# Optimization experiments

Hardware: AMD Instinct MI355X
Metric: run time of the kernel (lower is better)

## Reference

```python
import jax, jax.numpy as jnp
import numpy as np

N, K, C, G, B = 65536, 16, 64, 8, 4
PE_IN = 28  # 3 + 1 + 2*4*2 + 1*4*2
EPS = 1e-5
FREQS = (1.0, 2.0, 4.0, 8.0)  # 2 ** linspace(0, 3, 4)


def _bn(x, p):
    # inference-mode BatchNorm1d over last dim; p: [4, d] = (gamma, beta, mean, var)
    return (x - p[2]) * (p[0] / jnp.sqrt(p[3] + EPS)) + p[1]


def setup_inputs() -> dict:
    key = jax.random.key(0)
    ks = iter(jax.random.split(key, 48))

    def nrm(shape, s=0.05):
        return jax.random.normal(next(ks), shape, jnp.float32) * s

    def bnp(d):
        k1, k2, k3, k4 = jax.random.split(next(ks), 4)
        return jnp.stack([
            jax.random.uniform(k1, (d,), jnp.float32, 0.5, 1.5),   # gamma
            jax.random.normal(k2, (d,), jnp.float32) * 0.1,        # beta
            jax.random.normal(k3, (d,), jnp.float32) * 0.1,        # running mean
            jax.random.uniform(k4, (d,), jnp.float32, 0.5, 1.5),   # running var
        ])

    return dict(
        feat=nrm((N, C), 1.0),
        coord=jax.random.normal(next(ks), (N, 3), jnp.float32),
        reference_index=jax.random.randint(next(ks), (N, K), 0, N),
        offset=jnp.array([N // 4, N // 2, 3 * N // 4, N], dtype=jnp.int32),
        Wq=nrm((C, C)), bq=nrm((C,)), bnq=bnp(C),
        Wk=nrm((C, C)), bk=nrm((C,)), bnk=bnp(C),
        Wv=nrm((C, C)), bv=nrm((C,)),
        pe_W1=nrm((PE_IN, C)), pe_b1=nrm((C,)), pe_bn=bnp(C),
        pe_W2=nrm((C, C)), pe_b2=nrm((C,)),
        we_W1=nrm((C, G)), we_b1=nrm((G,)), we_bn=bnp(G),
        we_W2=nrm((G, G)), we_b2=nrm((G,)),
        cg_W1=nrm((3 * C, C)), cg_b1=nrm((C,)), cg_bn=bnp(C),
        cg_W2=nrm((C, G), 0.001), cg_b2=jnp.full((G,), 3.0, jnp.float32),
    )


def reference(feat, coord, reference_index, offset, Wq, bq, bnq, Wk, bk, bnk,
              Wv, bv, pe_W1, pe_b1, pe_bn, pe_W2, pe_b2,
              we_W1, we_b1, we_bn, we_W2, we_b2,
              cg_W1, cg_b1, cg_bn, cg_W2, cg_b2):
    n = feat.shape[0]
    q = jax.nn.relu(_bn(feat @ Wq + bq, bnq))          # [N, C]
    k = jax.nn.relu(_bn(feat @ Wk + bk, bnk))          # [N, C]
    v = feat @ Wv + bv                                 # [N, C]

    idx = reference_index                              # [N, K]; -1 = pad
    idx_safe = jnp.maximum(idx, 0)
    key_feat = k[idx_safe]                             # [N, K, C] gather
    neighbor_xyz = coord[idx_safe]                     # [N, K, 3]
    value_g = v[idx_safe]                              # [N, K, C]

    delta = neighbor_xyz - coord[:, None, :]           # [N, K, 3]
    # Anisotropic Fourier relative position encoding
    x = delta.reshape(-1, 3)
    d_xy, d_z = x[:, :2], x[:, 2:3]
    dist = jnp.linalg.norm(x, axis=1, keepdims=True)
    feats = [x, dist]
    for f in FREQS:
        feats += [jnp.sin(d_xy * (f * np.pi)), jnp.cos(d_xy * (f * np.pi))]
    for f in FREQS:
        feats += [jnp.sin(d_z * (f * np.pi)), jnp.cos(d_z * (f * np.pi))]
    xe = jnp.concatenate(feats, axis=1)                # [N*K, 28]
    rpe = jax.nn.relu(_bn(xe @ pe_W1 + pe_b1, pe_bn)) @ pe_W2 + pe_b2
    rpe = rpe.reshape(n, idx.shape[1], -1)             # [N, K, C]

    relation = key_feat - q[:, None, :] + rpe          # [N, K, C]
    geom_w = jax.nn.relu(_bn(relation @ we_W1 + we_b1, we_bn)) @ we_W2 + we_b2  # [N, K, G]

    neighbor_ctx = q[idx_safe].max(axis=1)             # [N, C]
    seg = jnp.searchsorted(offset, jnp.arange(n), side='right')
    seg_max = jax.ops.segment_max(q, seg, num_segments=offset.shape[0])
    global_ctx = seg_max[seg]                          # [N, C] offset-wise global max pool

    gate_in = jnp.concatenate([q, neighbor_ctx, global_ctx], axis=-1)  # [N, 3C]
    gate = jax.nn.sigmoid(
        jax.nn.relu(_bn(gate_in @ cg_W1 + cg_b1, cg_bn)) @ cg_W2 + cg_b2)  # [N, G]

    attn = jax.nn.softmax(geom_w * gate[:, None, :], axis=1)  # softmax over K
    mask = jnp.sign(idx + 1).astype(attn.dtype)        # [N, K]
    attn = attn * mask[:, :, None]

    vg = value_g.reshape(n, idx.shape[1], G, -1)       # [N, K, G, C//G]
    out = jnp.einsum('nkgi,nkg->ngi', vg, attn)
    return out.reshape(n, -1)
```

## Files before the change

### kernel.cpp

```cpp
#include <hip/hip_runtime.h>
#include <hip/hip_bf16.h>

#define EPSF 1e-5f

typedef __attribute__((ext_vector_type(8))) short short8;
typedef __attribute__((ext_vector_type(4))) float f32x4;

__device__ __forceinline__ int seg_of(int i, int o0, int o1, int o2) {
    return (i >= o0) + (i >= o1) + (i >= o2);
}

__device__ __forceinline__ unsigned short f2bf(float f) {
    unsigned int u = __float_as_uint(f);
    unsigned int r = (u + 0x7fffu + ((u >> 16) & 1u)) >> 16;
    return (unsigned short)r;
}
__device__ __forceinline__ unsigned int pack2bf(float a, float b) {
    return (unsigned int)f2bf(a) | ((unsigned int)f2bf(b) << 16);
}
__device__ __forceinline__ float bflo(unsigned int u) { return __uint_as_float(u << 16); }
__device__ __forceinline__ float bfhi(unsigned int u) { return __uint_as_float(u & 0xffff0000u); }

__device__ __forceinline__ void stage_rows_bf16(const unsigned short* __restrict__ src,
                                                unsigned short* dst, int l) {
    int row = l >> 2, cq = (l & 3) * 16;
    const short8* s = (const short8*)(src + (size_t)row*64 + cq);
    short8* d0 = (short8*)(dst + row*72 + cq);
    d0[0] = s[0];
    d0[1] = s[1];
}

__device__ __forceinline__ void stage_rows_f32(const float* __restrict__ src,
                                               unsigned short* dst, int l) {
    int row = l >> 2, cq = (l & 3) * 16;
    const float4* s = (const float4*)(src + (size_t)row*64 + cq);
    unsigned int* d = (unsigned int*)(dst + row*72 + cq);
    #pragma unroll
    for (int i = 0; i < 4; ++i) {
        float4 f = s[i];
        d[i*2]   = pack2bf(f.x, f.y);
        d[i*2+1] = pack2bf(f.z, f.w);
    }
}

__global__ __launch_bounds__(256) void k_prep(
    const float* __restrict__ pe_W1, const float* __restrict__ pe_b1, const float* __restrict__ pe_bn,
    const float* __restrict__ pe_W2, const float* __restrict__ pe_b2,
    const float* __restrict__ we_W1, const float* __restrict__ we_b1, const float* __restrict__ we_bn,
    const float* __restrict__ cg_W1, const float* __restrict__ cg_b1, const float* __restrict__ cg_bn,
    const float* __restrict__ Wq, const float* __restrict__ bq, const float* __restrict__ bnq,
    const float* __restrict__ Wk, const float* __restrict__ bk, const float* __restrict__ bnk,
    const float* __restrict__ Wv,
    float* __restrict__ peb1f, float* __restrict__ cvecg, float* __restrict__ cgb1f,
    float* __restrict__ biasqF, float* __restrict__ biaskF, float* __restrict__ cgW1cF,
    unsigned short* __restrict__ WqF, unsigned short* __restrict__ WkF, unsigned short* __restrict__ WvF,
    unsigned short* __restrict__ weW1F, unsigned short* __restrict__ cgW1aF,
    unsigned short* __restrict__ cgW1bF,
    unsigned short* __restrict__ W1frag, unsigned short* __restrict__ Wcfrag)
{
    int t = threadIdx.x;
    __shared__ float sc1[64], csc[64], sqv[64], skv[64], wsc[8], wsh[8];
    __shared__ float sWe[64][8], sWb[8], sWc[64][8];
    if (t < 64) {
        float g = pe_bn[t], b = pe_bn[64+t], m = pe_bn[128+t], v = pe_bn[192+t];
        float s = g / sqrtf(v + EPSF);
        sc1[t] = s; peb1f[t] = pe_b1[t]*s + (b - m*s);
        g = cg_bn[t]; b = cg_bn[64+t]; m = cg_bn[128+t]; v = cg_bn[192+t];
        s = g / sqrtf(v + EPSF);
        csc[t] = s; cgb1f[t] = cg_b1[t]*s + (b - m*s);
        g = bnq[t]; b = bnq[64+t]; m = bnq[128+t]; v = bnq[192+t];
        s = g / sqrtf(v + EPSF);
        sqv[t] = s; biasqF[t] = bq[t]*s + (b - m*s);
        g = bnk[t]; b = bnk[64+t]; m = bnk[128+t]; v = bnk[192+t];
        s = g / sqrtf(v + EPSF);
        skv[t] = s; biaskF[t] = bk[t]*s + (b - m*s);
    }
    if (t < 8) {
        float g = we_bn[t], b = we_bn[8+t], m = we_bn[16+t], v = we_bn[24+t];
        float s = g / sqrtf(v + EPSF);
        wsc[t] = s; wsh[t] = b - m*s;
    }
    __syncthreads();
    for (int u = t; u < 512; u += 256) { int g = u & 7; sWe[u >> 3][g] = we_W1[u] * wsc[g]; }
    if (t < 8) sWb[t] = we_b1[t] * wsc[t] + wsh[t];
    __syncthreads();
    for (int u = t; u < 512; u += 256) {
        int h = u >> 3, g = u & 7;
        float a = 0.f;
        for (int c = 0; c < 64; ++c) a += pe_W2[h*64 + c] * sWe[c][g];
        sWc[h][g] = a;
    }
    if (t < 8) {
        float a = sWb[t];
        for (int c = 0; c < 64; ++c) a += pe_b2[c] * sWe[c][t];
        cvecg[t] = a;
    }
    __syncthreads();
    for (int u = t; u < 4096; u += 256) {
        int tile = u >> 9, l = (u >> 3) & 63, j = u & 7;
        int col = (tile >> 1)*16 + (l & 15);
        int kk  = (tile & 1)*32 + (l >> 4)*8 + j;
        WqF[u]    = f2bf(Wq[kk*64 + col] * sqv[col]);
        WkF[u]    = f2bf(Wk[kk*64 + col] * skv[col]);
        WvF[u]    = f2bf(Wv[kk*64 + col]);
        cgW1aF[u] = f2bf(cg_W1[kk*64 + col] * csc[col]);
        cgW1bF[u] = f2bf(cg_W1[(64 + kk)*64 + col] * csc[col]);
    }
    for (int u = t; u < 1024; u += 256) {
        int tile = u >> 9, l = (u >> 3) & 63, j = u & 7;
        int col = l & 15;
        int kk  = tile*32 + (l >> 4)*8 + j;
        weW1F[u] = (col < 8) ? f2bf(sWe[kk][col]) : 0;
    }
    for (int u = t; u < 4096; u += 256) {
        int k = u >> 6, c = u & 63;
        cgW1cF[u] = cg_W1[(128 + k)*64 + c] * csc[c];
    }
    {
        int ct = t >> 6, l = t & 63;
        int col = 16*ct + (l & 15), kg = l >> 4;
        #pragma unroll
        for (int j = 0; j < 8; ++j) {
            int k = kg*8 + j;
            float v = (k < 28) ? pe_W1[k*64 + col] * sc1[col] : 0.f;
            W1frag[ct*512 + l*8 + j] = f2bf(v);
        }
    }
    if (t < 128) {
        int kg = t >> 6, l = t & 63, g = l & 15;
        #pragma unroll
        for (int j = 0; j < 8; ++j) {
            int k = kg*32 + (l >> 4)*8 + j;
            float v = (g < 8) ? sWc[k][g] : 0.f;
            Wcfrag[kg*512 + l*8 + j] = f2bf(v);
        }
    }
}

__global__ __launch_bounds__(256) void k_prep2(
    const float* __restrict__ cg_W2, const float* __restrict__ we_W2,
    unsigned short* __restrict__ cgW2F, unsigned short* __restrict__ W2frag)
{
    int t = threadIdx.x;
    for (int u = t; u < 1024; u += 256) {
        int tile = u >> 9, l = (u >> 3) & 63, j = u & 7;
        int col = l & 15;
        int kk  = tile*32 + (l >> 4)*8 + j;
        cgW2F[u] = (col < 8) ? f2bf(cg_W2[kk*8 + col]) : 0;
    }
    if (t < 64) {
        int l = t, g = l & 15;
        #pragma unroll
        for (int j = 0; j < 8; ++j) {
            float v = (l < 16 && g < 8) ? we_W2[j*8 + g] : 0.f;
            W2frag[l*8 + j] = f2bf(v);
        }
    }
}

__global__ __launch_bounds__(256) void k_qkv(
    const float* __restrict__ feat, const int* __restrict__ offs,
    const unsigned short* __restrict__ WqF, const unsigned short* __restrict__ WkF,
    const unsigned short* __restrict__ WvF, const unsigned short* __restrict__ weW1F,
    const float* __restrict__ biasqF, const float* __restrict__ biaskF,
    const float* __restrict__ bv,
    unsigned short* __restrict__ v_bf, unsigned short* __restrict__ q_bf,
    float* __restrict__ kw, float* __restrict__ qw, float* __restrict__ seg_max)
{
    __shared__ unsigned short sF[4][16*72];
    __shared__ unsigned short sQ[4][16*72];
    __shared__ unsigned short sK[4][16*72];
    __shared__ float sSeg[64];

    int t = threadIdx.x, w = t >> 6, l = t & 63;
    int lc = l & 15, lg = l >> 4;
    int rblk = blockIdx.x * 64;
    int r0 = rblk + w * 16;
    int o0 = offs[0], o1 = offs[1], o2 = offs[2];
    bool fast = seg_of(rblk, o0,o1,o2) == seg_of(rblk + 63, o0,o1,o2);

    if (t < 64) sSeg[t] = 0.f;
    __syncthreads();

    stage_rows_f32(feat + (size_t)r0*64, sF[w], l);
    short8 a0 = *(const short8*)(sF[w] + lc*72 + lg*8);
    short8 a1 = *(const short8*)(sF[w] + lc*72 + 32 + lg*8);

    float bqc[4], bkc[4], bvc[4];
    #pragma unroll
    for (int ct = 0; ct < 4; ++ct) {
        bqc[ct] = biasqF[ct*16 + lc];
        bkc[ct] = biaskF[ct*16 + lc];
        bvc[ct] = bv[ct*16 + lc];
    }

    #pragma unroll
    for (int ct = 0; ct < 4; ++ct) {
        f32x4 z = {0.f,0.f,0.f,0.f};
        short8 b0 = *(const short8*)(WqF + (ct*2+0)*512 + l*8);
        short8 b1 = *(const short8*)(WqF + (ct*2+1)*512 + l*8);
        f32x4 c = __builtin_amdgcn_mfma_f32_16x16x32_bf16(a0, b0, z, 0,0,0);
        c = __builtin_amdgcn_mfma_f32_16x16x32_bf16(a1, b1, c, 0,0,0);
        float cmax = 0.f;
        #pragma unroll
        for (int reg = 0; reg < 4; ++reg) {
            float qv = fmaxf(c[reg] + bqc[ct], 0.f);
            sQ[w][(lg*4 + reg)*72 + ct*16 + lc] = f2bf(qv);
            if (fast) cmax = fmaxf(cmax, qv);
            else atomicMax((unsigned int*)&seg_max[seg_of(r0 + lg*4 + reg,o0,o1,o2)*64 + ct*16 + lc],
                           __float_as_uint(qv));
        }
        if (fast) {
            cmax = fmaxf(cmax, __shfl_xor(cmax, 16));
            cmax = fmaxf(cmax, __shfl_xor(cmax, 32));
            if (lg == 0)
                atomicMax((unsigned int*)&sSeg[ct*16 + lc], __float_as_uint(cmax));
        }
    }
    #pragma unroll
    for (int ct = 0; ct < 4; ++ct) {
        f32x4 z = {0.f,0.f,0.f,0.f};
        short8 b0 = *(const short8*)(WkF + (ct*2+0)*512 + l*8);
        short8 b1 = *(const short8*)(WkF + (ct*2+1)*512 + l*8);
        f32x4 c = __builtin_amdgcn_mfma_f32_16x16x32_bf16(a0, b0, z, 0,0,0);
        c = __builtin_amdgcn_mfma_f32_16x16x32_bf16(a1, b1, c, 0,0,0);
        #pragma unroll
        for (int reg = 0; reg < 4; ++reg)
            sK[w][(lg*4 + reg)*72 + ct*16 + lc] = f2bf(fmaxf(c[reg] + bkc[ct], 0.f));
    }
    #pragma unroll
    for (int ct = 0; ct < 4; ++ct) {
        f32x4 z = {0.f,0.f,0.f,0.f};
        short8 b0 = *(const short8*)(WvF + (ct*2+0)*512 + l*8);
        short8 b1 = *(const short8*)(WvF + (ct*2+1)*512 + l*8);
        f32x4 c = __builtin_amdgcn_mfma_f32_16x16x32_bf16(a0, b0, z, 0,0,0);
        c = __builtin_amdgcn_mfma_f32_16x16x32_bf16(a1, b1, c, 0,0,0);
        #pragma unroll
        for (int reg = 0; reg < 4; ++reg)
            sF[w][(lg*4 + reg)*72 + ct*16 + lc] = f2bf(c[reg] + bvc[ct]);
    }
    {
        short8 wb0 = *(const short8*)(weW1F + l*8);
        short8 wb1 = *(const short8*)(weW1F + 512 + l*8);
        short8 aq0 = *(const short8*)(sQ[w] + lc*72 + lg*8);
        short8 aq1 = *(const short8*)(sQ[w] + lc*72 + 32 + lg*8);
        short8 ak0 = *(const short8*)(sK[w] + lc*72 + lg*8);
        short8 ak1 = *(const short8*)(sK[w] + lc*72 + 32 + lg*8);
        f32x4 z = {0.f,0.f,0.f,0.f};
        f32x4 cq = __builtin_amdgcn_mfma_f32_16x16x32_bf16(aq0, wb0, z, 0,0,0);
        cq = __builtin_amdgcn_mfma_f32_16x16x32_bf16(aq1, wb1, cq, 0,0,0);
        f32x4 ck = __builtin_amdgcn_mfma_f32_16x16x32_bf16(ak0, wb0, z, 0,0,0);
        ck = __builtin_amdgcn_mfma_f32_16x16x32_bf16(ak1, wb1, ck, 0,0,0);
        if (lc < 8) {
            #pragma unroll
            for (int reg = 0; reg < 4; ++reg) {
                qw[(size_t)(r0 + lg*4 + reg)*8 + lc] = cq[reg];
                kw[(size_t)(r0 + lg*4 + reg)*8 + lc] = ck[reg];
            }
        }
    }
    #pragma unroll
    for (int rep = 0; rep < 2; ++rep) {
        int row = (l >> 3) + rep*8;
        int ch = (l & 7) * 8;
        short8 vq = *(const short8*)(sQ[w] + row*72 + ch);
        *(short8*)(q_bf + (size_t)(r0 + row)*64 + ch) = vq;
        short8 vv = *(const short8*)(sF[w] + row*72 + ch);
        *(short8*)(v_bf + (size_t)(r0 + row)*64 + ch) = vv;
    }
    __syncthreads();
    if (fast && t < 64)
        atomicMax((unsigned int*)&seg_max[seg_of(rblk,o0,o1,o2)*64 + t],
                  __float_as_uint(sSeg[t]));
}

__global__ __launch_bounds__(256) void k_seg(
    const float* __restrict__ seg_max, const float* __restrict__ cgW1cF,
    const float* __restrict__ cgb1f, float* __restrict__ gseg2)
{
    int t = threadIdx.x;
    int c = t & 63, s = t >> 6;
    float a = cgb1f[c];
    for (int j = 0; j < 64; ++j) a += seg_max[s*64 + j] * cgW1cF[j*64 + c];
    gseg2[s*64 + c] = a;
}

__global__ __launch_bounds__(256, 3) void k_main(
    const float* __restrict__ coord, const int* __restrict__ ridx,
    const unsigned short* __restrict__ v_bf, const unsigned short* __restrict__ q_bf,
    const float* __restrict__ kw, const float* __restrict__ qw,
    const float* __restrict__ peb1f, const float* __restrict__ cvecg,
    const float* __restrict__ we_b2, const float* __restrict__ cg_b2,
    const float* __restrict__ gseg2, const int* __restrict__ offs,
    const unsigned short* __restrict__ W1frag, const unsigned short* __restrict__ Wcfrag,
    const unsigned short* __restrict__ W2frag,
    const unsigned short* __restrict__ cgW1aF, const unsigned short* __restrict__ cgW1bF,
    const unsigned short* __restrict__ cgW2F,
    float* __restrict__ out)
{
    __shared__ __align__(16) unsigned short sA1[256*40];
    __shared__ __align__(16) unsigned short sA2[4][16*72];
    __shared__ __align__(16) unsigned short sAh2[4][128];
    __shared__ float sAttn[4][4][16][9];
    __shared__ int sIds[256];
    __shared__ __align__(16) unsigned short sQg[16*72];
    __shared__ __align__(16) unsigned short sN[16*72];
    __shared__ __align__(16) unsigned short sHg[16*72];
    __shared__ float sGate[16][9];

    int t = threadIdx.x, w = t >> 6, l = t & 63;
    int lc = l & 15, lg = l >> 4;
    int n0 = blockIdx.x * 16;
    int o0 = offs[0], o1 = offs[1], o2 = offs[2];

    int id = ridx[(size_t)n0*16 + t];
    sIds[t] = id;
    int ids = max(id, 0);
    int nself = n0 + (t >> 4);
    {
        float cx = coord[nself*3], cy = coord[nself*3+1], cz = coord[nself*3+2];
        float dx = coord[ids*3]   - cx;
        float dy = coord[ids*3+1] - cy;
        float dz = coord[ids*3+2] - cz;
        float dist = sqrtf(dx*dx + dy*dy + dz*dz);
        unsigned int* row = (unsigned int*)sA1 + t*20;
        row[0] = pack2bf(dx, dy);
        row[1] = pack2bf(dz, dist);
        float sx, cx2, sy, cy2, sz, cz2;
        __sincosf(dx * 3.14159265358979f, &sx, &cx2);
        __sincosf(dy * 3.14159265358979f, &sy, &cy2);
        __sincosf(dz * 3.14159265358979f, &sz, &cz2);
        row[2]  = pack2bf(sx, sy);
        row[3]  = pack2bf(cx2, cy2);
        row[10] = pack2bf(sz, cz2);
        #pragma unroll
        for (int fi = 1; fi < 4; ++fi) {
            float nsx = 2.f*sx*cx2, ncx = fmaf(-2.f*sx, sx, 1.f);
            float nsy = 2.f*sy*cy2, ncy = fmaf(-2.f*sy, sy, 1.f);
            float nsz = 2.f*sz*cz2, ncz = fmaf(-2.f*sz, sz, 1.f);
            row[2 + 2*fi] = pack2bf(nsx, nsy);
            row[3 + 2*fi] = pack2bf(ncx, ncy);
            row[10 + fi]  = pack2bf(nsz, ncz);
            sx = nsx; cx2 = ncx; sy = nsy; cy2 = ncy; sz = nsz; cz2 = ncz;
        }
        row[14] = 0u; row[15] = 0u;
    }
    if (t < 64) stage_rows_bf16(q_bf + (size_t)n0*64, sQg, t);
    __syncthreads();

    {
        int p = t >> 4, s = t & 15;
        const int* ip = &sIds[p*16];
        float m0 = 0.f, m1 = 0.f, m2 = 0.f, m3 = 0.f;
        #pragma unroll
        for (int kb = 0; kb < 16; kb += 4) {
            uint2 u[4];
            #pragma unroll
            for (int j = 0; j < 4; ++j) {
                int idn = max(ip[kb + j], 0);
                u[j] = *(const uint2*)(q_bf + (size_t)idn*64 + s*4);
            }
            #pragma unroll
            for (int j = 0; j < 4; ++j) {
                m0 = fmaxf(m0, bflo(u[j].x)); m1 = fmaxf(m1, bfhi(u[j].x));
                m2 = fmaxf(m2, bflo(u[j].y)); m3 = fmaxf(m3, bfhi(u[j].y));
            }
        }
        unsigned int* d = (unsigned int*)(sN + p*72 + s*4);
        d[0] = pack2bf(m0, m1);
        d[1] = pack2bf(m2, m3);
    }
    __syncthreads();

    {
        short8 a0 = *(const short8*)(sQg + lc*72 + lg*8);
        short8 a1 = *(const short8*)(sQg + lc*72 + 32 + lg*8);
        short8 nv0 = *(const short8*)(sN + lc*72 + lg*8);
        short8 nv1 = *(const short8*)(sN + lc*72 + 32 + lg*8);
        f32x4 c4;
        #pragma unroll
        for (int reg = 0; reg < 4; ++reg)
            c4[reg] = gseg2[seg_of(n0 + lg*4 + reg, o0, o1, o2)*64 + w*16 + lc];
        short8 b0 = *(const short8*)(cgW1aF + (w*2+0)*512 + l*8);
        short8 b1 = *(const short8*)(cgW1aF + (w*2+1)*512 + l*8);
        c4 = __builtin_amdgcn_mfma_f32_16x16x32_bf16(a0, b0, c4, 0,0,0);
        c4 = __builtin_amdgcn_mfma_f32_16x16x32_bf16(a1, b1, c4, 0,0,0);
        short8 b2 = *(const short8*)(cgW1bF + (w*2+0)*512 + l*8);
        short8 b3 = *(const short8*)(cgW1bF + (w*2+1)*512 + l*8);
        c4 = __builtin_amdgcn_mfma_f32_16x16x32_bf16(nv0, b2, c4, 0,0,0);
        c4 = __builtin_amdgcn_mfma_f32_16x16x32_bf16(nv1, b3, c4, 0,0,0);
        #pragma unroll
        for (int reg = 0; reg < 4; ++reg)
            sHg[(lg*4 + reg)*72 + w*16 + lc] = f2bf(fmaxf(c4[reg], 0.f));
    }
    __syncthreads();

    if (w == 0) {
        short8 ah0 = *(const short8*)(sHg + lc*72 + lg*8);
        short8 ah1 = *(const short8*)(sHg + lc*72 + 32 + lg*8);
        short8 w0f = *(const short8*)(cgW2F + l*8);
        short8 w1f = *(const short8*)(cgW2F + 512 + l*8);
        float bg = cg_b2[lc & 7];
        f32x4 cg;
        #pragma unroll
        for (int reg = 0; reg < 4; ++reg) cg[reg] = bg;
        cg = __builtin_amdgcn_mfma_f32_16x16x32_bf16(ah0, w0f, cg, 0,0,0);
        cg = __builtin_amdgcn_mfma_f32_16x16x32_bf16(ah1, w1f, cg, 0,0,0);
        if (lc < 8) {
            #pragma unroll
            for (int reg = 0; reg < 4; ++reg)
                sGate[lg*4 + reg][lc] = 1.f / (1.f + __expf(-cg[reg]));
        }
    }
    __syncthreads();

    int g7 = lc & 7;
    short8 bW1[4], bWc[2], bW2;
    #pragma unroll
    for (int ct = 0; ct < 4; ++ct) bW1[ct] = *(const short8*)(W1frag + ct*512 + l*8);
    bWc[0] = *(const short8*)(Wcfrag + l*8);
    bWc[1] = *(const short8*)(Wcfrag + 512 + l*8);
    bW2 = *(const short8*)(W2frag + l*8);

    float bias1[4];
    #pragma unroll
    for (int ct = 0; ct < 4; ++ct) bias1[ct] = peb1f[16*ct + lc];
    float cvec_g = cvecg[g7];
    float bias3 = we_b2[g7];

    #pragma unroll
    for (int rt = 0; rt < 4; ++rt) {
        int n = n0 + w*4 + rt;
        short8 a1 = *(const short8*)(sA1 + (w*64 + rt*16 + lc)*40 + lg*8);
        f32x4 c1[4];
        #pragma unroll
        for (int ct = 0; ct < 4; ++ct) {
            f32x4 z = {0.f, 0.f, 0.f, 0.f};
            c1[ct] = __builtin_amdgcn_mfma_f32_16x16x32_bf16(a1, bW1[ct], z, 0, 0, 0);
        }
        #pragma unroll
        for (int ct = 0; ct < 4; ++ct) {
            #pragma unroll
            for (int reg = 0; reg < 4; ++reg) {
                float h1 = fmaxf(c1[ct][reg] + bias1[ct], 0.f);
                sA2[w][(lg*4 + reg)*72 + 16*ct + lc] = f2bf(h1);
            }
        }
        int ids_r[4];
        #pragma unroll
        for (int reg = 0; reg < 4; ++reg) ids_r[reg] = sIds[w*64 + rt*16 + lg*4 + reg];
        float qwv = qw[(size_t)n*8 + g7];
        f32x4 c2;
        #pragma unroll
        for (int reg = 0; reg < 4; ++reg)
            c2[reg] = kw[(size_t)max(ids_r[reg],0)*8 + g7] - qwv + cvec_g;
        short8 a20 = *(const short8*)(sA2[w] + lc*72 + lg*8);
        short8 a21 = *(const short8*)(sA2[w] + lc*72 + 32 + lg*8);
        c2 = __builtin_amdgcn_mfma_f32_16x16x32_bf16(a20, bWc[0], c2, 0, 0, 0);
        c2 = __builtin_amdgcn_mfma_f32_16x16x32_bf16(a21, bWc[1], c2, 0, 0, 0);
        if (lc < 8) {
            #pragma unroll
            for (int reg = 0; reg < 4; ++reg)
                sAh2[w][(lg*4 + reg)*8 + lc] = f2bf(fmaxf(c2[reg], 0.f));
        }
        short8 a3 = {0,0,0,0,0,0,0,0};
        if (l < 16) a3 = *(const short8*)(sAh2[w] + lc*8);
        f32x4 c3;
        #pragma unroll
        for (int reg = 0; reg < 4; ++reg) c3[reg] = bias3;
        c3 = __builtin_amdgcn_mfma_f32_16x16x32_bf16(a3, bW2, c3, 0, 0, 0);
        float gv = sGate[w*4 + rt][g7];
        float lgt[4];
        #pragma unroll
        for (int reg = 0; reg < 4; ++reg) lgt[reg] = c3[reg] * gv;
        float m = fmaxf(fmaxf(lgt[0], lgt[1]), fmaxf(lgt[2], lgt[3]));
        m = fmaxf(m, __shfl_xor(m, 16));
        m = fmaxf(m, __shfl_xor(m, 32));
        float e[4], s = 0.f;
        #pragma unroll
        for (int reg = 0; reg < 4; ++reg) { e[reg] = __expf(lgt[reg] - m); s += e[reg]; }
        s += __shfl_xor(s, 16);
        s += __shfl_xor(s, 32);
        float inv = 1.f / s;
        if (lc < 8) {
            #pragma unroll
            for (int reg = 0; reg < 4; ++reg) {
                int idv = ids_r[reg];
                float mf = (idv >= 0) ? 1.f : ((idv == -1) ? 0.f : -1.f);
                sAttn[w][rt][lg*4 + reg][lc] = e[reg] * inv * mf;
            }
        }
    }

    {
        int p = lg, kk = lc;
        int n2 = n0 + w*4 + p;
        float4 o = make_float4(0.f, 0.f, 0.f, 0.f);
        int gh = kk >> 1;
        #pragma unroll
        for (int k2 = 0; k2 < 16; ++k2) {
            int id2 = max(sIds[w*64 + p*16 + k2], 0);
            float a = sAttn[w][p][k2][gh];
            uint2 u = *(const uint2*)(v_bf + (size_t)id2*64 + kk*4);
            o.x += a * bflo(u.x); o.y += a * bfhi(u.x);
            o.z += a * bflo(u.y); o.w += a * bfhi(u.y);
        }
        *(float4*)(out + (size_t)n2*64 + kk*4) = o;
    }
}

extern "C" void kernel_launch(void* const* d_in, const int* in_sizes, int n_in,
                              void* d_out, int out_size, void* d_ws, size_t ws_size,
                              hipStream_t stream)
{
    const float* feat  = (const float*)d_in[0];
    const float* coord = (const float*)d_in[1];
    const int*   ridx  = (const int*)d_in[2];
    const int*   offs  = (const int*)d_in[3];
    const float* Wq = (const float*)d_in[4];  const float* bq = (const float*)d_in[5];  const float* bnq = (const float*)d_in[6];
    const float* Wk = (const float*)d_in[7];  const float* bk = (const float*)d_in[8];  const float* bnk = (const float*)d_in[9];
    const float* Wv = (const float*)d_in[10]; const float* bv = (const float*)d_in[11];
    const float* pe_W1 = (const float*)d_in[12]; const float* pe_b1 = (const float*)d_in[13]; const float* pe_bn = (const float*)d_in[14];
    const float* pe_W2 = (const float*)d_in[15]; const float* pe_b2 = (const float*)d_in[16];
    const float* we_W1 = (const float*)d_in[17]; const float* we_b1 = (const float*)d_in[18]; const float* we_bn = (const float*)d_in[19];
    const float* we_W2 = (const float*)d_in[20]; const float* we_b2 = (const float*)d_in[21];
    const float* cg_W1 = (const float*)d_in[22]; const float* cg_b1 = (const float*)d_in[23]; const float* cg_bn = (const float*)d_in[24];
    const float* cg_W2 = (const float*)d_in[25]; const float* cg_b2 = (const float*)d_in[26];
    float* out = (float*)d_out;
    int N = in_sizes[0] / 64;

    unsigned short* v_bf = (unsigned short*)d_ws;
    unsigned short* q_bf = v_bf + (size_t)N*64;
    float* kwp   = (float*)(q_bf + (size_t)N*64);
    float* qwp   = kwp + (size_t)N*8;
    float* gatep = qwp + (size_t)N*8;
    float* segm  = gatep + (size_t)N*8;
    float* gseg2 = segm + 256;
    float* peb1f = gseg2 + 256;
    float* cvecg = peb1f + 64;
    float* cgb1f = cvecg + 8;
    float* biasqF= cgb1f + 64;
    float* biaskF= biasqF + 64;
    float* pad0  = biaskF + 64;
    float* cgW1cF= pad0 + 56;
    unsigned short* WqF     = (unsigned short*)(cgW1cF + 4096);
    unsigned short* WkF     = WqF + 4096;
    unsigned short* WvF     = WkF + 4096;
    unsigned short* weW1F   = WvF + 4096;
    unsigned short* cgW1aF  = weW1F + 1024;
    unsigned short* cgW1bF  = cgW1aF + 4096;
    unsigned short* cgW2F   = cgW1bF + 4096;
    unsigned short* W1frag  = cgW2F + 1024;
    unsigned short* Wcfrag  = W1frag + 2048;
    unsigned short* W2frag  = Wcfrag + 1024;

    hipMemsetAsync(segm, 0, 256 * sizeof(float), stream);
    k_prep<<<1, 256, 0, stream>>>(pe_W1, pe_b1, pe_bn, pe_W2, pe_b2,
                                  we_W1, we_b1, we_bn,
                                  cg_W1, cg_b1, cg_bn,
                                  Wq, bq, bnq, Wk, bk, bnk, Wv,
                                  peb1f, cvecg, cgb1f, biasqF, biaskF, cgW1cF,
                                  WqF, WkF, WvF, weW1F, cgW1aF, cgW1bF,
                                  W1frag, Wcfrag);
    k_prep2<<<1, 256, 0, stream>>>(cg_W2, we_W2, cgW2F, W2frag);
    k_qkv<<<N/64, 256, 0, stream>>>(feat, offs, WqF, WkF, WvF, weW1F,
                                    biasqF, biaskF, bv,
                                    v_bf, q_bf, kwp, qwp, segm);
    k_seg<<<1, 256, 0, stream>>>(segm, cgW1cF, cgb1f, gseg2);
    k_main<<<N/16, 256, 0, stream>>>(coord, ridx, v_bf, q_bf, kwp, qwp,
                                     peb1f, cvecg, we_b2, cg_b2, gseg2, offs,
                                     W1frag, Wcfrag, W2frag,
                                     cgW1aF, cgW1bF, cgW2F, out);
}
```

Before: 111.7 us.

## Merge prep kernels, alias main-kernel LDS buffers, raise occupancy target

Folds k_prep2 into k_prep so one fewer kernel launches, and moves the per-block segment-max atomic flush earlier in k_qkv. In k_main, several LDS buffers (sQg, sN, sHg, the per-wave activation scratch and attention weights) are aliased into a single union buffer, and attention weights are stored as bf16. This cuts shared memory so the launch bound can rise from 3 to 4 blocks per SM. The trade-offs are tighter register pressure and bf16 rounding of the attention weights, plus the risk of overlapping lifetimes in the aliased buffers.

```diff
diff --git a/kernel.cpp b/kernel.cpp
--- a/kernel.cpp
+++ b/kernel.cpp
@@ -47,7 +47,9 @@
     const float* __restrict__ pe_W1, const float* __restrict__ pe_b1, const float* __restrict__ pe_bn,
     const float* __restrict__ pe_W2, const float* __restrict__ pe_b2,
     const float* __restrict__ we_W1, const float* __restrict__ we_b1, const float* __restrict__ we_bn,
+    const float* __restrict__ we_W2,
     const float* __restrict__ cg_W1, const float* __restrict__ cg_b1, const float* __restrict__ cg_bn,
+    const float* __restrict__ cg_W2,
     const float* __restrict__ Wq, const float* __restrict__ bq, const float* __restrict__ bnq,
     const float* __restrict__ Wk, const float* __restrict__ bk, const float* __restrict__ bnk,
     const float* __restrict__ Wv,
@@ -55,8 +57,9 @@
     float* __restrict__ biasqF, float* __restrict__ biaskF, float* __restrict__ cgW1cF,
     unsigned short* __restrict__ WqF, unsigned short* __restrict__ WkF, unsigned short* __restrict__ WvF,
     unsigned short* __restrict__ weW1F, unsigned short* __restrict__ cgW1aF,
-    unsigned short* __restrict__ cgW1bF,
-    unsigned short* __restrict__ W1frag, unsigned short* __restrict__ Wcfrag)
+    unsigned short* __restrict__ cgW1bF, unsigned short* __restrict__ cgW2F,
+    unsigned short* __restrict__ W1frag, unsigned short* __restrict__ Wcfrag,
+    unsigned short* __restrict__ W2frag)
 {
     int t = threadIdx.x;
     __shared__ float sc1[64], csc[64], sqv[64], skv[64], wsc[8], wsh[8];
@@ -111,6 +114,7 @@
         int col = l & 15;
         int kk  = tile*32 + (l >> 4)*8 + j;
         weW1F[u] = (col < 8) ? f2bf(sWe[kk][col]) : 0;
+        cgW2F[u] = (col < 8) ? f2bf(cg_W2[kk*8 + col]) : 0;
     }
     for (int u = t; u < 4096; u += 256) {
         int k = u >> 6, c = u & 63;
@@ -134,19 +138,6 @@
             float v = (g < 8) ? sWc[k][g] : 0.f;
             Wcfrag[kg*512 + l*8 + j] = f2bf(v);
         }
-    }
-}
-
-__global__ __launch_bounds__(256) void k_prep2(
-    const float* __restrict__ cg_W2, const float* __restrict__ we_W2,
-    unsigned short* __restrict__ cgW2F, unsigned short* __restrict__ W2frag)
-{
-    int t = threadIdx.x;
-    for (int u = t; u < 1024; u += 256) {
-        int tile = u >> 9, l = (u >> 3) & 63, j = u & 7;
-        int col = l & 15;
-        int kk  = tile*32 + (l >> 4)*8 + j;
-        cgW2F[u] = (col < 8) ? f2bf(cg_W2[kk*8 + col]) : 0;
     }
     if (t < 64) {
         int l = t, g = l & 15;
@@ -217,6 +208,11 @@
                 atomicMax((unsigned int*)&sSeg[ct*16 + lc], __float_as_uint(cmax));
         }
     }
+    __syncthreads();
+    if (fast && t < 64)
+        atomicMax((unsigned int*)&seg_max[seg_of(rblk,o0,o1,o2)*64 + t],
+                  __float_as_uint(sSeg[t]));
+
     #pragma unroll
     for (int ct = 0; ct < 4; ++ct) {
         f32x4 z = {0.f,0.f,0.f,0.f};
@@ -268,10 +264,6 @@
         short8 vv = *(const short8*)(sF[w] + row*72 + ch);
         *(short8*)(v_bf + (size_t)(r0 + row)*64 + ch) = vv;
     }
-    __syncthreads();
-    if (fast && t < 64)
-        atomicMax((unsigned int*)&seg_max[seg_of(rblk,o0,o1,o2)*64 + t],
-                  __float_as_uint(sSeg[t]));
 }
 
 __global__ __launch_bounds__(256) void k_seg(
@@ -285,7 +277,7 @@
     gseg2[s*64 + c] = a;
 }
 
-__global__ __launch_bounds__(256, 3) void k_main(
+__global__ __launch_bounds__(256, 4) void k_main(
     const float* __restrict__ coord, const int* __restrict__ ridx,
     const unsigned short* __restrict__ v_bf, const unsigned short* __restrict__ q_bf,
     const float* __restrict__ kw, const float* __restrict__ qw,
@@ -300,18 +292,20 @@
 {
     __shared__ __align__(16) unsigned short sA1[256*40];
     __shared__ __align__(16) unsigned short sA2[4][16*72];
-    __shared__ __align__(16) unsigned short sAh2[4][128];
-    __shared__ float sAttn[4][4][16][9];
+    __shared__ __align__(16) unsigned short sU[3456];
+    __shared__ float sGate[16][9];
     __shared__ int sIds[256];
-    __shared__ __align__(16) unsigned short sQg[16*72];
-    __shared__ __align__(16) unsigned short sN[16*72];
-    __shared__ __align__(16) unsigned short sHg[16*72];
-    __shared__ float sGate[16][9];
 
     int t = threadIdx.x, w = t >> 6, l = t & 63;
     int lc = l & 15, lg = l >> 4;
     int n0 = blockIdx.x * 16;
     int o0 = offs[0], o1 = offs[1], o2 = offs[2];
+
+    unsigned short* sQg = sU;
+    unsigned short* sN  = sU + 1152;
+    unsigned short* sHg = sU + 2304;
+    unsigned short* sAh2w  = sU + w*128;
+    unsigned short* sAttnB = sU + 512;
 
     int id = ridx[(size_t)n0*16 + t];
     sIds[t] = id;
@@ -461,10 +455,10 @@
         if (lc < 8) {
             #pragma unroll
             for (int reg = 0; reg < 4; ++reg)
-                sAh2[w][(lg*4 + reg)*8 + lc] = f2bf(fmaxf(c2[reg], 0.f));
+                sAh2w[(lg*4 + reg)*8 + lc] = f2bf(fmaxf(c2[reg], 0.f));
         }
         short8 a3 = {0,0,0,0,0,0,0,0};
-        if (l < 16) a3 = *(const short8*)(sAh2[w] + lc*8);
+        if (l < 16) a3 = *(const short8*)(sAh2w + lc*8);
         f32x4 c3;
         #pragma unroll
         for (int reg = 0; reg < 4; ++reg) c3[reg] = bias3;
@@ -487,7 +481,7 @@
             for (int reg = 0; reg < 4; ++reg) {
                 int idv = ids_r[reg];
                 float mf = (idv >= 0) ? 1.f : ((idv == -1) ? 0.f : -1.f);
-                sAttn[w][rt][lg*4 + reg][lc] = e[reg] * inv * mf;
+                sAttnB[((w*4 + rt)*16 + lg*4 + reg)*8 + lc] = f2bf(e[reg] * inv * mf);
             }
         }
     }
@@ -500,7 +494,7 @@
         #pragma unroll
         for (int k2 = 0; k2 < 16; ++k2) {
             int id2 = max(sIds[w*64 + p*16 + k2], 0);
-            float a = sAttn[w][p][k2][gh];
+            float a = bflo((unsigned int)sAttnB[((w*4 + p)*16 + k2)*8 + gh]);
             uint2 u = *(const uint2*)(v_bf + (size_t)id2*64 + kk*4);
             o.x += a * bflo(u.x); o.y += a * bfhi(u.x);
             o.z += a * bflo(u.y); o.w += a * bfhi(u.y);
@@ -556,13 +550,12 @@
 
     hipMemsetAsync(segm, 0, 256 * sizeof(float), stream);
     k_prep<<<1, 256, 0, stream>>>(pe_W1, pe_b1, pe_bn, pe_W2, pe_b2,
-                                  we_W1, we_b1, we_bn,
-                                  cg_W1, cg_b1, cg_bn,
+                                  we_W1, we_b1, we_bn, we_W2,
+                                  cg_W1, cg_b1, cg_bn, cg_W2,
                                   Wq, bq, bnq, Wk, bk, bnk, Wv,
                                   peb1f, cvecg, cgb1f, biasqF, biaskF, cgW1cF,
-                                  WqF, WkF, WvF, weW1F, cgW1aF, cgW1bF,
-                                  W1frag, Wcfrag);
-    k_prep2<<<1, 256, 0, stream>>>(cg_W2, we_W2, cgW2F, W2frag);
+                                  WqF, WkF, WvF, weW1F, cgW1aF, cgW1bF, cgW2F,
+                                  W1frag, Wcfrag, W2frag);
     k_qkv<<<N/64, 256, 0, stream>>>(feat, offs, WqF, WkF, WvF, weW1F,
                                     biasqF, biaskF, bv,
                                     v_bf, q_bf, kwp, qwp, segm);
```

After: 105.1 us (median of 2 runs). 6.0% less time.
